# Optimization experiments

Measured on AMD Instinct MI355X. Metric: run time of the kernel, lower is better.

The kernel has to match this reference:

```python
import jax, jax.numpy as jnp
import numpy as np

B, IMG, TXT, N, FF, HID, C, E = 1024, 512, 300, 14, 2048, 128, 14, 182
D = IMG + TXT  # 812, transformer d_model


def setup_inputs() -> dict:
    key = jax.random.key(0)
    ks = jax.random.split(key, 12)
    r = lambda k, s, sc=0.02: (jax.random.normal(k, s, jnp.float32) * sc)
    return {
        "img_feat": jax.random.normal(ks[0], (B, IMG), jnp.float32),
        "word_embeds": jax.random.normal(ks[1], (N, TXT), jnp.float32),
        "edge_index": jax.random.randint(ks[2], (2, E), 0, N, jnp.int32),
        "in_proj_w": r(ks[3], (3 * D, D)),
        "in_proj_b": jnp.zeros((3 * D,), jnp.float32),
        "out_proj_w": r(ks[4], (D, D)),
        "out_proj_b": jnp.zeros((D,), jnp.float32),
        "ln1_g": jnp.ones((D,), jnp.float32), "ln1_b": jnp.zeros((D,), jnp.float32),
        "ln2_g": jnp.ones((D,), jnp.float32), "ln2_b": jnp.zeros((D,), jnp.float32),
        "ffn_w1": r(ks[5], (D, FF)), "ffn_b1": jnp.zeros((FF,), jnp.float32),
        "ffn_w2": r(ks[6], (FF, D)), "ffn_b2": jnp.zeros((D,), jnp.float32),
        "gcn1_w": r(ks[7], (D, HID)), "gcn1_b": jnp.zeros((HID,), jnp.float32),
        "gcn2_w": r(ks[8], (HID, HID)), "gcn2_b": jnp.zeros((HID,), jnp.float32),
        "lin_w": r(ks[9], (HID, C)), "lin_b": jnp.zeros((C,), jnp.float32),
    }


def layer_norm(x, g, b, eps=1e-5):
    mu = x.mean(-1, keepdims=True)
    var = ((x - mu) ** 2).mean(-1, keepdims=True)
    return (x - mu) * jax.lax.rsqrt(var + eps) * g + b


def gcn_conv(x, edge_index, W, b, n_nodes):
    # PyG GCNConv: add self loops, symmetric normalization, x @ W then scatter-add.
    # x: (B, N, F_in); gather/scatter along node axis (node_dim=-2).
    src, dst = edge_index[0], edge_index[1]
    loop = jnp.arange(n_nodes, dtype=src.dtype)
    src = jnp.concatenate([src, loop])
    dst = jnp.concatenate([dst, loop])
    deg = jnp.zeros((n_nodes,), x.dtype).at[dst].add(1.0)
    dinv = jnp.where(deg > 0, deg ** -0.5, 0.0)
    ew = dinv[src] * dinv[dst]                       # (E+N,)
    h = x @ W                                        # (B, N, F_out)
    msg = h[:, src, :] * ew[None, :, None]           # gather neighbors
    out = jnp.zeros_like(h).at[:, dst, :].add(msg)   # scatter-aggregate
    return out + b


def reference(img_feat, word_embeds, edge_index,
              in_proj_w, in_proj_b, out_proj_w, out_proj_b,
              ln1_g, ln1_b, ln2_g, ln2_b,
              ffn_w1, ffn_b1, ffn_w2, ffn_b2,
              gcn1_w, gcn1_b, gcn2_w, gcn2_b, lin_w, lin_b):
    # Broadcast image feature across the 14 label nodes; concat word embeddings.
    node = jnp.concatenate([
        jnp.broadcast_to(img_feat[:, None, :], (B, N, IMG)),
        jnp.broadcast_to(word_embeds[None, :, :], (B, N, TXT)),
    ], axis=-1)                                      # (B, N, D)

    # torch TransformerEncoderLayer, batch_first=False, nhead=1, post-norm, relu.
    # Input (B, N, D) is interpreted as (seq=B, batch=N, D): attention over dim 0.
    qkv = node @ in_proj_w.T + in_proj_b
    q, k, v = jnp.split(qkv, 3, axis=-1)             # each (B, N, D)
    scale = 1.0 / jnp.sqrt(jnp.asarray(D, node.dtype))
    scores = jnp.einsum('lnd,mnd->nlm', q, k) * scale  # (N, B, B)
    attn = jax.nn.softmax(scores, axis=-1)
    ao = jnp.einsum('nlm,mnd->lnd', attn, v)           # (B, N, D)
    ao = ao @ out_proj_w.T + out_proj_b
    x = layer_norm(node + ao, ln1_g, ln1_b)
    ff = jax.nn.relu(x @ ffn_w1 + ffn_b1) @ ffn_w2 + ffn_b2
    x = layer_norm(x + ff, ln2_g, ln2_b)               # (B, N, D)

    # Two GCNConv layers over the 14-node label graph (batched over B).
    x = jax.nn.relu(gcn_conv(x, edge_index, gcn1_w, gcn1_b, N))
    x = gcn_conv(x, edge_index, gcn2_w, gcn2_b, N)
    x = jax.nn.relu(x.mean(axis=1))                    # mean over nodes -> (B, HID)
    return x @ lin_w + lin_b                           # (B, C)
```

## Files before the change

kernel.cpp:

```cpp
#include <hip/hip_runtime.h>
#include <math.h>

#define B_    1024
#define IMG_  512
#define TXT_  300
#define NN_   14
#define FF_   2048
#define HID_  128
#define CC_   14
#define EE_   182
#define DD_   812
#define D3_   2436
#define BNR_  14336
#define KP_   832
#define TXP_  320
#define AROWS_ 1152

typedef __bf16 bf16x8 __attribute__((ext_vector_type(8)));
typedef float  f32x4  __attribute__((ext_vector_type(4)));
typedef unsigned short u16;

__device__ __forceinline__ u16 f2bf(float f) {
    union { float f; unsigned u; } v; v.f = f;
    unsigned r = v.u + 0x7FFFu + ((v.u >> 16) & 1u);
    return (u16)(r >> 16);
}
__device__ __forceinline__ float bf2f(u16 h) {
    union { unsigned u; float f; } v; v.u = ((unsigned)h) << 16; return v.f;
}

__device__ __forceinline__ void gload_lds16(const u16* g, u16* l) {
    __builtin_amdgcn_global_load_lds(
        (const __attribute__((address_space(1))) void*)g,
        (__attribute__((address_space(3))) void*)l, 16, 0, 0);
}

#define OFF_IMGB  0ULL
#define OFF_WIB   1048576ULL
#define OFF_WORDB 3543040ULL
#define OFF_WITX  3624960ULL
#define OFF_GB    0ULL
#define OFF_EBUF  29360128ULL
#define OFF_AVOT  33611776ULL
#define OFF_WOB   35446784ULL
#define OFF_HB    0ULL
#define OFF_PB    58720256ULL
#define OFF_X1B   82001920ULL
#define OFF_YB    105857024ULL
#define OFF_W1T   129712128ULL
#define OFF_W2T   133120000ULL
#define OFF_AQB   152420352ULL
#define OFF_TVB   158307552ULL
#define OFF_CO    158520544ULL
#define OFF_Z     158566016ULL
#define OFF_ADJ   158623360ULL
#define OFF_WG1T  158624384ULL
#define OFF_WG2T  158837376ULL

__device__ __forceinline__ void gemm_epi(
    float v, int rm, int cn, int epi,
    float* __restrict__ Cf, int ldc, u16* __restrict__ Cb, int ldcb,
    const float* __restrict__ bias)
{
    if (epi == 0) Cf[(size_t)rm * ldc + cn] = v;
    else if (epi == 1) { v += bias[cn]; v = v > 0.f ? v : 0.f;
                    Cb[(size_t)rm * ldcb + cn] = f2bf(v); }
    else if (epi == 2) Cf[(size_t)rm * ldc + cn] =
                    v + bias[cn] + bf2f(Cb[(size_t)rm * ldcb + cn]);
    else if (epi == 3) Cb[(size_t)rm * ldcb + cn] = f2bf(v);
    else if (epi == 4) { int bs = cn / DD_, cc = cn - bs * DD_;
                    Cb[(size_t)bs * (AROWS_ * KP_) + (size_t)rm * KP_ + cc] = f2bf(v); }
    else if (epi == 5) { float invz = 1.0f / bias[rm];
                    Cb[(size_t)rm * ldcb + cn] = f2bf(v * invz); }
    else if (epi == 6) Cf[(size_t)rm * ldc + cn] = v + bias[cn];
    else if (epi == 7) { const u16* rx = (const u16*)Cf;
                    Cb[(size_t)rm * ldcb + cn] =
                        f2bf(v + bias[cn] + bf2f(rx[(size_t)rm * ldc + cn])); }
    else if (epi == 8) {
        float t = v + bias[cn];
        if (cn < DD_) Cb[(size_t)(1024 + rm) * KP_ + cn] = f2bf(t);
        else if (cn >= 2 * DD_)
            ((u16*)Cf)[(size_t)rm * KP_ + (cn - 2 * DD_)] = f2bf(t);
    }
}

__device__ __forceinline__ void gemm256_body(
    const u16* __restrict__ A, int lda,
    const u16* __restrict__ Bm, int ldb,
    int M, int N, int K, float scale,
    float* __restrict__ Cf, int ldc,
    u16* __restrict__ Cb, int ldcb,
    const float* __restrict__ bias,
    int nxt, int epi, int id)
{
    __shared__ __align__(16) u16 As[4][8192];
    __shared__ __align__(16) u16 Bs[4][8192];
    const int tid = threadIdx.x;
    const int bx = id % nxt, by = id / nxt;
    const int row0 = by << 8, col0 = bx << 8;
    const int lane = tid & 63, wv = tid >> 6;
    const int wm = (wv >> 2) << 7;
    const int wn = (wv & 3) << 6;
    const int fr = lane & 15, qd = lane >> 4;

    int aoff[8], boff[4];
    #pragma unroll
    for (int mi = 0; mi < 8; ++mi) {
        int r = wm + mi * 16 + fr;
        aoff[mi] = r * 32 + ((qd ^ ((r >> 1) & 3)) << 3);
    }
    #pragma unroll
    for (int ni = 0; ni < 4; ++ni) {
        int r = wn + ni * 16 + fr;
        boff[ni] = r * 32 + ((qd ^ ((r >> 1) & 3)) << 3);
    }

    const int i0 = tid, i1 = 512 + tid;
    const int r0 = i0 >> 2, r1 = i1 >> 2;
    const int c0 = ((i0 & 3) ^ ((r0 >> 1) & 3)) << 3;
    const int c1 = ((i1 & 3) ^ ((r1 >> 1) & 3)) << 3;
    const u16* Ag0 = A  + (size_t)(row0 + r0) * lda + c0;
    const u16* Ag1 = A  + (size_t)(row0 + r1) * lda + c1;
    const u16* Bg0 = Bm + (size_t)(col0 + r0) * ldb + c0;
    const u16* Bg1 = Bm + (size_t)(col0 + r1) * ldb + c1;
    const int lb0 = wv * 512;
    const int lb1 = 4096 + wv * 512;

    f32x4 acc[8][4] = {};
    const int T = K >> 5;

    #pragma unroll
    for (int p = 0; p < 3; ++p) {
        const int ko = p << 5;
        gload_lds16(Ag0 + ko, &As[p][lb0]);
        gload_lds16(Ag1 + ko, &As[p][lb1]);
        gload_lds16(Bg0 + ko, &Bs[p][lb0]);
        gload_lds16(Bg1 + ko, &Bs[p][lb1]);
    }
    __builtin_amdgcn_sched_barrier(0);
    asm volatile("s_waitcnt vmcnt(8)");
    __builtin_amdgcn_sched_barrier(0);
    __builtin_amdgcn_s_barrier();
    __builtin_amdgcn_sched_barrier(0);

    for (int t = 0; t < T; ++t) {
        const int slot = t & 3;
        const u16* as = &As[slot][0];
        const u16* bs = &Bs[slot][0];
        const int ns = (t + 3) & 3;
        const int ko = (t + 3) << 5;
        const bool pf = (t + 3 < T);

        bf16x8 a[8];
        #pragma unroll
        for (int mi = 0; mi < 8; ++mi)
            a[mi] = *(const bf16x8*)(as + aoff[mi]);
        bf16x8 b0 = *(const bf16x8*)(bs + boff[0]);
        bf16x8 b1 = *(const bf16x8*)(bs + boff[1]);
        if (pf) {
            gload_lds16(Ag0 + ko, &As[ns][lb0]);
            gload_lds16(Ag1 + ko, &As[ns][lb1]);
        }
        __builtin_amdgcn_sched_barrier(0);
        __builtin_amdgcn_s_barrier();
        __builtin_amdgcn_sched_barrier(0);
        __builtin_amdgcn_s_setprio(1);
        #pragma unroll
        for (int mi = 0; mi < 8; ++mi) {
            acc[mi][0] = __builtin_amdgcn_mfma_f32_16x16x32_bf16(
                a[mi], b0, acc[mi][0], 0, 0, 0);
            acc[mi][1] = __builtin_amdgcn_mfma_f32_16x16x32_bf16(
                a[mi], b1, acc[mi][1], 0, 0, 0);
        }
        __builtin_amdgcn_s_setprio(0);
        __builtin_amdgcn_sched_barrier(0);
        __builtin_amdgcn_s_barrier();
        __builtin_amdgcn_sched_barrier(0);

        bf16x8 b2 = *(const bf16x8*)(bs + boff[2]);
        bf16x8 b3 = *(const bf16x8*)(bs + boff[3]);
        if (pf) {
            gload_lds16(Bg0 + ko, &Bs[ns][lb0]);
            gload_lds16(Bg1 + ko, &Bs[ns][lb1]);
        }
        __builtin_amdgcn_sched_barrier(0);
        if (t < T - 3) asm volatile("s_waitcnt vmcnt(8)");
        else           asm volatile("s_waitcnt vmcnt(0)");
        __builtin_amdgcn_sched_barrier(0);
        __builtin_amdgcn_s_barrier();
        __builtin_amdgcn_sched_barrier(0);
        __builtin_amdgcn_s_setprio(1);
        #pragma unroll
        for (int mi = 0; mi < 8; ++mi) {
            acc[mi][2] = __builtin_amdgcn_mfma_f32_16x16x32_bf16(
                a[mi], b2, acc[mi][2], 0, 0, 0);
            acc[mi][3] = __builtin_amdgcn_mfma_f32_16x16x32_bf16(
                a[mi], b3, acc[mi][3], 0, 0, 0);
        }
        __builtin_amdgcn_s_setprio(0);
        __builtin_amdgcn_sched_barrier(0);
        __builtin_amdgcn_s_barrier();
        __builtin_amdgcn_sched_barrier(0);
    }

    #pragma unroll
    for (int mi = 0; mi < 8; ++mi) {
        #pragma unroll
        for (int i = 0; i < 4; ++i) {
            int rm = row0 + wm + mi * 16 + qd * 4 + i;
            if (rm >= M) continue;
            #pragma unroll
            for (int ni = 0; ni < 4; ++ni) {
                int cn = col0 + wn + ni * 16 + fr;
                if (cn >= N) continue;
                gemm_epi(acc[mi][ni][i] * scale, rm, cn, epi, Cf, ldc, Cb, ldcb, bias);
            }
        }
    }
}

template<int EPI>
__global__ __launch_bounds__(512, 2)
void bgemm256(const u16* __restrict__ A, int lda,
              const u16* __restrict__ Bm, int ldb,
              int M, int N, int K, float scale,
              float* __restrict__ Cf, int ldc,
              u16* __restrict__ Cb, int ldcb,
              const float* __restrict__ bias,
              int nxt)
{
    const int g8 = (int)gridDim.x >> 3;
    const int id = (int)blockIdx.x;
    const int w = (id & 7) * g8 + (id >> 3);
    gemm256_body(A, lda, Bm, ldb, M, N, K, scale, Cf, ldc, Cb, ldcb, bias,
                 nxt, EPI, w);
}

__device__ __forceinline__ void gemm_body8(
    const u16* __restrict__ A, int lda,
    const u16* __restrict__ Bm, int ldb,
    int M, int N, int K, float scale,
    float* __restrict__ Cf, int ldc,
    u16* __restrict__ Cb, int ldcb,
    const float* __restrict__ bias,
    int nxt, int swiz, int epi, int id)
{
    __shared__ __align__(16) u16 As[2][128 * 32];
    __shared__ __align__(16) u16 Bs[2][128 * 32];
    const int tid = threadIdx.x;
    int bx, by;
    if (swiz) { int r8 = id & 7; int q = id >> 3; bx = q % nxt; by = (q / nxt) * 8 + r8; }
    else      { bx = id % nxt; by = id / nxt; }
    const int row0 = by * 128, col0 = bx * 128;
    const int lane = tid & 63, wv = tid >> 6;
    const int wm = (wv >> 1) * 32, wn = (wv & 1) * 64;
    const int fr = lane & 15, qd = lane >> 4;

    const int s_b0  = wv * 512;
    const int s_row = tid >> 2;
    const int s_ko  = (tid & 3) * 8;
    const u16* Arow = A  + (size_t)(row0 + s_row) * lda + s_ko;
    const u16* Brow = Bm + (size_t)(col0 + s_row) * ldb + s_ko;

    f32x4 acc[2][4] = {};

    const int T = K >> 5;
    gload_lds16(Arow, &As[0][s_b0]);
    gload_lds16(Brow, &Bs[0][s_b0]);

    for (int i = 0; i < T; ++i) {
        __syncthreads();
        const int cur = i & 1;
        if (i + 1 < T) {
            const int ko = (i + 1) << 5;
            gload_lds16(Arow + ko, &As[cur ^ 1][s_b0]);
            gload_lds16(Brow + ko, &Bs[cur ^ 1][s_b0]);
        }
        bf16x8 af[2], bg[4];
        #pragma unroll
        for (int j = 0; j < 2; ++j)
            af[j] = *(const bf16x8*)&As[cur][(wm + j * 16 + fr) * 32 + qd * 8];
        #pragma unroll
        for (int j = 0; j < 4; ++j)
            bg[j] = *(const bf16x8*)&Bs[cur][(wn + j * 16 + fr) * 32 + qd * 8];
        #pragma unroll
        for (int mi = 0; mi < 2; ++mi)
            #pragma unroll
            for (int ni = 0; ni < 4; ++ni)
                acc[mi][ni] = __builtin_amdgcn_mfma_f32_16x16x32_bf16(
                    af[mi], bg[ni], acc[mi][ni], 0, 0, 0);
    }

    #pragma unroll
    for (int mi = 0; mi < 2; ++mi) {
        #pragma unroll
        for (int i = 0; i < 4; ++i) {
            int rm = row0 + wm + mi * 16 + qd * 4 + i;
            if (rm >= M) continue;
            #pragma unroll
            for (int ni = 0; ni < 4; ++ni) {
                int cn = col0 + wn + ni * 16 + fr;
                if (cn >= N) continue;
                gemm_epi(acc[mi][ni][i] * scale, rm, cn, epi, Cf, ldc, Cb, ldcb, bias);
            }
        }
    }
}

struct GDesc {
    const u16* A; const u16* B; float* Cf; u16* Cb; const float* bias;
    int lda, ldb, ldc, ldcb, M, N, K, epi, nxt, swiz, blk0;
    float scale;
};
struct TDesc { const float* src; u16* dst; int srs, drs, rows, cols, padrows, rt, nblk; };
struct MPack { GDesc g[3]; TDesc t[2]; const int* ei; float* Adj; int ng, gtot, nt; };

__device__ __forceinline__ void castT_body(TDesc T, int id)
{
    __shared__ float t[32][33];
    const int bx = id % T.rt, by = id / T.rt;
    const int r0 = bx * 32, c0 = by * 32;
    const int tx = threadIdx.x & 31, ty = threadIdx.x >> 5;
    #pragma unroll
    for (int k = 0; k < 2; ++k) {
        int r = r0 + ty + k * 16, c = c0 + tx;
        t[ty + k * 16][tx] = (r < T.rows && c < T.cols) ? T.src[(size_t)r * T.srs + c] : 0.f;
    }
    __syncthreads();
    #pragma unroll
    for (int k = 0; k < 2; ++k) {
        int c = c0 + ty + k * 16, r = r0 + tx;
        if (c < T.cols && r < T.padrows)
            T.dst[(size_t)c * T.drs + r] = f2bf(t[tx][ty + k * 16]);
    }
}

__device__ __forceinline__ void adj_body(const int* __restrict__ ei, float* __restrict__ Adj)
{
    __shared__ float degS[NN_], dinvS[NN_], adjS[NN_ * NN_];
    const int tid = threadIdx.x;
    if (tid < NN_) degS[tid] = 1.f;
    if (tid < NN_ * NN_) adjS[tid] = 0.f;
    __syncthreads();
    int s = 0, d = 0;
    if (tid < EE_) { s = ei[tid]; d = ei[EE_ + tid]; atomicAdd(&degS[d], 1.f); }
    __syncthreads();
    if (tid < NN_) dinvS[tid] = rsqrtf(degS[tid]);
    __syncthreads();
    if (tid < EE_) atomicAdd(&adjS[d * NN_ + s], dinvS[s] * dinvS[d]);
    if (tid < NN_) atomicAdd(&adjS[tid * NN_ + tid], dinvS[tid] * dinvS[tid]);
    __syncthreads();
    if (tid < NN_ * NN_) Adj[tid] = adjS[tid];
    if (tid < 16) {
        float sum = 0.f;
        if (tid < NN_)
            for (int j = 0; j < NN_; ++j) sum += adjS[j * NN_ + tid];
        Adj[NN_ * NN_ + tid] = sum / (float)NN_;
    }
}

__global__ __launch_bounds__(512, 6)
void kern_mix(MPack p)
{
    int id = blockIdx.x;
    if (id < p.gtot) {
        int si = 0;
        for (int s = 1; s < p.ng; ++s) if (id >= p.g[s].blk0) si = s;
        GDesc D = p.g[si];
        gemm_body8(D.A, D.lda, D.B, D.ldb, D.M, D.N, D.K, D.scale,
                   D.Cf, D.ldc, D.Cb, D.ldcb, D.bias, D.nxt, D.swiz, D.epi,
                   id - D.blk0);
        return;
    }
    id -= p.gtot;
    for (int s = 0; s < p.nt; ++s) {
        if (id < p.t[s].nblk) { castT_body(p.t[s], id); return; }
        id -= p.t[s].nblk;
    }
    if (id == 0 && p.ei) adj_body(p.ei, p.Adj);
}

struct CDesc { const float* src; u16* dst; int srs, drs, dcols, scols; };
struct CPack { CDesc d[9]; unsigned cum[10]; int n; };

__global__ void kern_mcast(CPack p)
{
    unsigned idx = blockIdx.x * 256 + threadIdx.x;
    int si = -1;
    for (int s = 0; s < p.n; ++s)
        if (idx >= p.cum[s] && idx < p.cum[s + 1]) { si = s; break; }
    if (si < 0) return;
    CDesc D = p.d[si];
    unsigned k = idx - p.cum[si];
    int r = k / D.dcols, c = k - r * D.dcols;
    D.dst[(size_t)r * D.drs + c] =
        (c < D.scols) ? f2bf(D.src[(size_t)r * D.srs + c]) : (u16)0;
}

__global__ __launch_bounds__(256) void kern_eG(const float* __restrict__ S,
    u16* __restrict__ Gb, float* __restrict__ Z)
{
    __shared__ float red[256];
    __shared__ u16 ews[NN_ * 1024];
    const int l = blockIdx.x, tid = threadIdx.x;
    const int lane = tid & 63, wv = tid >> 6;

    const float* wraw = S + 1024 * 1024;
    for (int z = wv; z < NN_; z += 4) {
        const float* r = wraw + z * 1024;
        float vv[16], mx = -1e30f;
        #pragma unroll
        for (int j = 0; j < 16; ++j) { vv[j] = r[lane + 64 * j]; mx = fmaxf(mx, vv[j]); }
        #pragma unroll
        for (int off = 32; off > 0; off >>= 1) mx = fmaxf(mx, __shfl_down(mx, off));
        mx = __shfl(mx, 0);
        #pragma unroll
        for (int j = 0; j < 16; ++j)
            ews[z * 1024 + lane + 64 * j] = f2bf(expf(vv[j] - mx));
    }
    const float* row = S + (size_t)l * 1024;
    float m = -1e30f;
    #pragma unroll
    for (int k = 0; k < 4; ++k) m = fmaxf(m, row[tid + 256 * k]);
    red[tid] = m; __syncthreads();
    for (int s = 128; s > 0; s >>= 1) {
        if (tid < s) red[tid] = fmaxf(red[tid], red[tid + s]);
        __syncthreads();
    }
    m = red[0];
    float ev[16];
    #pragma unroll
    for (int j = 0; j < 16; ++j) ev[j] = expf(row[lane + 64 * j] - m);
    u16* gr = Gb + (size_t)l * NN_ * 1024;
    for (int z = wv; z < NN_; z += 4) {
        const u16* er = &ews[z * 1024];
        float s = 0.f;
        #pragma unroll
        for (int j = 0; j < 16; ++j) {
            float pv = ev[j] * bf2f(er[lane + 64 * j]);
            gr[(size_t)z * 1024 + lane + 64 * j] = f2bf(pv);
            s += pv;
        }
        #pragma unroll
        for (int off = 32; off > 0; off >>= 1) s += __shfl_down(s, off);
        if (lane == 0) Z[l * NN_ + z] = s;
    }
}

__global__ __launch_bounds__(256) void kern_ln1(
    const float* __restrict__ img, const float* __restrict__ word,
    const u16* __restrict__ Pb,
    const float* __restrict__ co, const float* __restrict__ g,
    const float* __restrict__ bta, u16* __restrict__ Xb)
{
    __shared__ float buf[DD_];
    __shared__ float red[256];
    __shared__ float stats[2];
    int row = blockIdx.x;
    int b = row / NN_, n = row - b * NN_;
    const u16* pr = Pb + (size_t)row * DD_;
    const float* cr = co + n * DD_;
    float s = 0.f;
    for (int d = threadIdx.x; d < DD_; d += 256) {
        float v = (d < IMG_) ? img[(size_t)b * IMG_ + d] : word[n * TXT_ + d - IMG_];
        v += bf2f(pr[d]) + cr[d];
        buf[d] = v; s += v;
    }
    red[threadIdx.x] = s; __syncthreads();
    for (int t = 128; t > 0; t >>= 1) {
        if (threadIdx.x < t) red[threadIdx.x] += red[threadIdx.x + t];
        __syncthreads();
    }
    if (threadIdx.x == 0) stats[0] = red[0] / DD_;
    __syncthreads();
    float mu = stats[0], s2 = 0.f;
    for (int d = threadIdx.x; d < DD_; d += 256) { float t = buf[d] - mu; s2 += t * t; }
    red[threadIdx.x] = s2; __syncthreads();
    for (int t = 128; t > 0; t >>= 1) {
        if (threadIdx.x < t) red[threadIdx.x] += red[threadIdx.x + t];
        __syncthreads();
    }
    if (threadIdx.x == 0) stats[1] = rsqrtf(red[0] / DD_ + 1e-5f);
    __syncthreads();
    float rstd = stats[1];
    u16* xb = Xb + (size_t)row * KP_;
    for (int d = threadIdx.x; d < DD_; d += 256)
        xb[d] = f2bf((buf[d] - mu) * rstd * g[d] + bta[d]);
    for (int d = DD_ + threadIdx.x; d < KP_; d += 256) xb[d] = 0;
}

#define X2S_ 840
#define G1S_ 136
__global__ __launch_bounds__(256, 4)
void kern_gcn(const u16* __restrict__ Yb,
              const float* __restrict__ g2v, const float* __restrict__ bt2,
              const u16* __restrict__ Wg1T, const float* __restrict__ bg1,
              const u16* __restrict__ Wg2T, const float* __restrict__ bg2,
              const float* __restrict__ Wl,  const float* __restrict__ bl,
              const float* __restrict__ AdjW, float* __restrict__ out)
{
    __shared__ __align__(16) u16 x2s[16 * X2S_];
    __shared__ __align__(16) float h1s[16 * 132];
    __shared__ float adj_s[NN_ * NN_];
    __shared__ float colw_s[16];
    __shared__ float pool_s[HID_];
    u16* g1s = x2s;
    const int b = blockIdx.x, tid = threadIdx.x;
    const int lane = tid & 63, wv = tid >> 6;
    const int fr = lane & 15, qd = lane >> 4;

    if (tid < NN_ * NN_) adj_s[tid] = AdjW[tid];
    if (tid >= NN_ * NN_ && tid < NN_ * NN_ + 16) colw_s[tid - NN_ * NN_] = AdjW[tid];
    for (int k = tid; k < 2 * X2S_; k += 256) x2s[14 * X2S_ + k] = 0;
    for (int k = tid; k < 14 * (X2S_ - DD_); k += 256) {
        int j = k / (X2S_ - DD_), c = k - j * (X2S_ - DD_);
        x2s[j * X2S_ + DD_ + c] = 0;
    }

    for (int j = wv; j < NN_; j += 4) {
        const u16* yr = Yb + (size_t)(b * NN_ + j) * KP_;
        float vv[13], s = 0.f;
        #pragma unroll
        for (int k = 0; k < 13; ++k) {
            int d = lane + 64 * k;
            float v = (d < DD_) ? bf2f(yr[d]) : 0.f;
            vv[k] = v; s += v;
        }
        #pragma unroll
        for (int off = 32; off > 0; off >>= 1) s += __shfl_down(s, off);
        s = __shfl(s, 0);
        float mu = s / (float)DD_, s2 = 0.f;
        #pragma unroll
        for (int k = 0; k < 13; ++k) {
            int d = lane + 64 * k;
            float t = (d < DD_) ? vv[k] - mu : 0.f;
            s2 += t * t;
        }
        #pragma unroll
        for (int off = 32; off > 0; off >>= 1) s2 += __shfl_down(s2, off);
        s2 = __shfl(s2, 0);
        float rstd = rsqrtf(s2 / (float)DD_ + 1e-5f);
        #pragma unroll
        for (int k = 0; k < 13; ++k) {
            int d = lane + 64 * k;
            if (d < DD_)
                x2s[j * X2S_ + d] = f2bf((vv[k] - mu) * rstd * g2v[d] + bt2[d]);
        }
    }
    __syncthreads();

    {
        f32x4 acc[2] = {{}, {}};
        const u16* wp0 = Wg1T + (size_t)(wv * 32 + fr) * KP_ + qd * 8;
        const u16* wp1 = wp0 + (size_t)16 * KP_;
        bf16x8 bc0 = *(const bf16x8*)wp0;
        bf16x8 bc1 = *(const bf16x8*)wp1;
        for (int k0 = 0; k0 < KP_; k0 += 32) {
            bf16x8 bn0 = bc0, bn1 = bc1;
            if (k0 + 32 < KP_) {
                bn0 = *(const bf16x8*)(wp0 + k0 + 32);
                bn1 = *(const bf16x8*)(wp1 + k0 + 32);
            }
            bf16x8 af = *(const bf16x8*)&x2s[fr * X2S_ + k0 + qd * 8];
            acc[0] = __builtin_amdgcn_mfma_f32_16x16x32_bf16(af, bc0, acc[0], 0, 0, 0);
            acc[1] = __builtin_amdgcn_mfma_f32_16x16x32_bf16(af, bc1, acc[1], 0, 0, 0);
            bc0 = bn0; bc1 = bn1;
        }
        #pragma unroll
        for (int t = 0; t < 2; ++t)
            #pragma unroll
            for (int i = 0; i < 4; ++i)
                h1s[(qd * 4 + i) * 132 + wv * 32 + t * 16 + fr] = acc[t][i];
    }
    __syncthreads();

    {
        const int f = tid & 127, jj = (tid >> 7) * 7;
        #pragma unroll
        for (int j = 0; j < 7; ++j) {
            float s = bg1[f];
            #pragma unroll
            for (int i = 0; i < NN_; ++i)
                s = fmaf(adj_s[(jj + j) * NN_ + i], h1s[i * 132 + f], s);
            g1s[(jj + j) * G1S_ + f] = f2bf(s > 0.f ? s : 0.f);
        }
        for (int k = tid; k < 2 * G1S_; k += 256) g1s[14 * G1S_ + k] = 0;
    }
    __syncthreads();

    {
        f32x4 acc[2] = {{}, {}};
        const u16* wp0 = Wg2T + (size_t)(wv * 32 + fr) * HID_ + qd * 8;
        const u16* wp1 = wp0 + (size_t)16 * HID_;
        bf16x8 bc0 = *(const bf16x8*)wp0;
        bf16x8 bc1 = *(const bf16x8*)wp1;
        for (int k0 = 0; k0 < HID_; k0 += 32) {
            bf16x8 bn0 = bc0, bn1 = bc1;
            if (k0 + 32 < HID_) {
                bn0 = *(const bf16x8*)(wp0 + k0 + 32);
                bn1 = *(const bf16x8*)(wp1 + k0 + 32);
            }
            bf16x8 af = *(const bf16x8*)&g1s[fr * G1S_ + k0 + qd * 8];
            acc[0] = __builtin_amdgcn_mfma_f32_16x16x32_bf16(af, bc0, acc[0], 0, 0, 0);
            acc[1] = __builtin_amdgcn_mfma_f32_16x16x32_bf16(af, bc1, acc[1], 0, 0, 0);
            bc0 = bn0; bc1 = bn1;
        }
        #pragma unroll
        for (int t = 0; t < 2; ++t) {
            float s = 0.f;
            #pragma unroll
            for (int i = 0; i < 4; ++i) s += colw_s[qd * 4 + i] * acc[t][i];
            s += __shfl_xor(s, 16);
            s += __shfl_xor(s, 32);
            if (qd == 0) {
                int f = wv * 32 + t * 16 + fr;
                float p = s + bg2[f];
                pool_s[f] = p > 0.f ? p : 0.f;
            }
        }
    }
    __syncthreads();

    if (tid < CC_) {
        float s = bl[tid];
        #pragma unroll 8
        for (int f = 0; f < HID_; ++f)
            s = fmaf(pool_s[f], Wl[(size_t)f * CC_ + tid], s);
        out[(size_t)b * CC_ + tid] = s;
    }
}

extern "C" void kernel_launch(void* const* d_in, const int* in_sizes, int n_in,
                              void* d_out, int out_size, void* d_ws, size_t ws_size,
                              hipStream_t stream)
{
    const float* img  = (const float*)d_in[0];
    const float* word = (const float*)d_in[1];
    const int*   ei   = (const int*)d_in[2];
    const float* Wi   = (const float*)d_in[3];
    const float* bi   = (const float*)d_in[4];
    const float* Wo   = (const float*)d_in[5];
    const float* bo   = (const float*)d_in[6];
    const float* g1   = (const float*)d_in[7];
    const float* bt1  = (const float*)d_in[8];
    const float* g2   = (const float*)d_in[9];
    const float* bt2  = (const float*)d_in[10];
    const float* W1   = (const float*)d_in[11];
    const float* bf1  = (const float*)d_in[12];
    const float* W2   = (const float*)d_in[13];
    const float* bf2  = (const float*)d_in[14];
    const float* Wg1  = (const float*)d_in[15];
    const float* bg1  = (const float*)d_in[16];
    const float* Wg2  = (const float*)d_in[17];
    const float* bg2  = (const float*)d_in[18];
    const float* Wl   = (const float*)d_in[19];
    const float* bl   = (const float*)d_in[20];
    float* out = (float*)d_out;

    char* ws = (char*)d_ws;
    u16*   imgb = (u16*)  (ws + OFF_IMGB);
    u16*   Wib  = (u16*)  (ws + OFF_WIB);
    u16*   wordb= (u16*)  (ws + OFF_WORDB);
    u16*   WiTX = (u16*)  (ws + OFF_WITX);
    u16*   Gb   = (u16*)  (ws + OFF_GB);
    float* Ebuf = (float*)(ws + OFF_EBUF);
    u16*   AvoT = (u16*)  (ws + OFF_AVOT);
    u16*   Wob  = (u16*)  (ws + OFF_WOB);
    u16*   Hb   = (u16*)  (ws + OFF_HB);
    u16*   Pb   = (u16*)  (ws + OFF_PB);
    u16*   X1b  = (u16*)  (ws + OFF_X1B);
    u16*   Yb   = (u16*)  (ws + OFF_YB);
    u16*   W1T  = (u16*)  (ws + OFF_W1T);
    u16*   W2T  = (u16*)  (ws + OFF_W2T);
    u16*   Aqb  = (u16*)  (ws + OFF_AQB);
    u16*   Akb  = Aqb + AROWS_ * KP_;
    u16*   Avb  = Aqb + 2 * AROWS_ * KP_;
    u16*   Tvb  = (u16*)  (ws + OFF_TVB);
    float* co   = (float*)(ws + OFF_CO);
    float* Zb   = (float*)(ws + OFF_Z);
    float* Adj  = (float*)(ws + OFF_ADJ);
    u16*   Wg1T = (u16*)  (ws + OFF_WG1T);
    u16*   Wg2T = (u16*)  (ws + OFF_WG2T);

    const float scl = 1.0f / sqrtf((float)DD_);

    {
        CPack p; p.n = 9;
        unsigned c = 0;
        auto seg = [&](int i, const float* s, int srs, u16* d, int drs,
                       int rows, int dcols, int scols) {
            p.d[i] = { s, d, srs, drs, dcols, scols };
            p.cum[i] = c; c += (unsigned)rows * dcols;
        };
        seg(0, img,        IMG_, imgb,  IMG_, B_,   IMG_, IMG_);
        seg(1, Wi,         DD_,  Wib,   IMG_, D3_,  IMG_, IMG_);
        seg(2, word,       TXT_, wordb, TXP_, NN_,  TXP_, TXT_);
        seg(3, Wi + IMG_,  DD_,  WiTX,  TXP_, D3_,  TXP_, TXT_);
        seg(4, Wo,         DD_,  Wob,   KP_,  DD_,  KP_,  DD_);
        seg(5, nullptr, 0, Aqb + DD_,                    KP_, 1038, 20, 0);
        seg(6, nullptr, 0, Aqb + AROWS_ * KP_ + DD_,     KP_, 1024, 20, 0);
        seg(7, nullptr, 0, Aqb + 2 * AROWS_ * KP_ + DD_, KP_, 1024, 20, 0);
        seg(8, nullptr, 0, Tvb + DD_,                    KP_, NN_,  20, 0);
        p.cum[9] = c;
        kern_mcast<<<(c + 255) / 256, 256, 0, stream>>>(p);
    }

    {
        MPack p{};
        p.ng = 2; p.gtot = 180;
        p.g[0] = { wordb, WiTX, (float*)Tvb, Aqb, bi,
                   TXP_, TXP_, 0, 0, NN_, D3_, TXP_, 8, 20, 0, 0, 1.f };
        p.g[1] = { imgb, Wib, nullptr, Aqb, nullptr,
                   IMG_, IMG_, 0, 0, B_, D3_, IMG_, 4, 20, 1, 20, 1.f };
        p.nt = 2;
        p.t[0] = { Wg1, Wg1T, HID_, KP_,  DD_,  HID_, KP_,  26, 26 * 4 };
        p.t[1] = { Wg2, Wg2T, HID_, HID_, HID_, HID_, HID_, 4,  4 * 4 };
        p.ei = ei; p.Adj = Adj;
        kern_mix<<<180 + 104 + 16 + 1, 512, 0, stream>>>(p);
    }

    {
        MPack p{};
        p.ng = 3; p.gtot = 135;
        p.g[0] = { Aqb, Akb, Ebuf, nullptr, nullptr,
                   KP_, KP_, 1024, 0, 1024 + NN_, 1024, KP_, 0, 8, 0, 0, scl };
        p.g[1] = { Wob, Avb, nullptr, AvoT, nullptr,
                   KP_, KP_, 0, 1024, DD_, B_, KP_, 3, 8, 0, 72, 1.f };
        p.g[2] = { Tvb, Wob, co, nullptr, bo,
                   KP_, KP_, DD_, 0, NN_, DD_, KP_, 6, 7, 0, 128, 1.f };
        p.nt = 2;
        p.t[0] = { W1, W1T, FF_, KP_, DD_, FF_, KP_, 26, 26 * 64 };
        p.t[1] = { W2, W2T, DD_, FF_, FF_, DD_, FF_, 64, 64 * 26 };
        p.ei = nullptr; p.Adj = nullptr;
        kern_mix<<<135 + 1664 + 1664, 512, 0, stream>>>(p);
    }

    kern_eG<<<1024, 256, 0, stream>>>(Ebuf, Gb, Zb);

    bgemm256<5><<<56 * 4, 512, 0, stream>>>(Gb, 1024, AvoT, 1024,
        BNR_, DD_, 1024, 1.f, nullptr, 0, Pb, DD_, Zb, 4);

    kern_ln1<<<BNR_, 256, 0, stream>>>(img, word, Pb, co, g1, bt1, X1b);

    bgemm256<1><<<56 * 8, 512, 0, stream>>>(X1b, KP_, W1T, KP_,
        BNR_, FF_, KP_, 1.f, nullptr, 0, Hb, FF_, bf1, 8);
    bgemm256<7><<<56 * 4, 512, 0, stream>>>(Hb, FF_, W2T, FF_,
        BNR_, DD_, FF_, 1.f, (float*)X1b, KP_, Yb, KP_, bf2, 4);

    kern_gcn<<<B_, 256, 0, stream>>>(Yb, g2, bt2, Wg1T, bg1, Wg2T, bg2,
                                     Wl, bl, Adj, out);
}
```

Measured before the change: 478.4 us.

## Add 128x128 double-buffered GEMM with grouped tile swizzle for attention-out and FFN1

Adds a new 128x128-tile MFMA GEMM kernel with 256 threads, two LDS buffers of 32-wide K slices, and an optional row-grouped block swizzle that improves L2 reuse. The attention-value GEMM and the first FFN GEMM now use it instead of the 256x256 kernel. The aim is to launch more blocks for better occupancy and load balance across CUs, since the 256-tile grid of 224 or 448 blocks may underfill the device. The cost is less data reuse per tile and more global traffic. The FFN2 GEMM keeps the old kernel.

After: 459.4 us. 4.0% less time.

```diff
diff --git a/kernel.cpp b/kernel.cpp
--- a/kernel.cpp
+++ b/kernel.cpp
@@ -82,6 +82,97 @@
         else if (cn >= 2 * DD_)
             ((u16*)Cf)[(size_t)rm * KP_ + (cn - 2 * DD_)] = f2bf(t);
     }
+}
+
+__device__ __forceinline__ void gemm_body4(
+    const u16* __restrict__ A, int lda,
+    const u16* __restrict__ Bm, int ldb,
+    int M, int N, int K, float scale,
+    float* __restrict__ Cf, int ldc,
+    u16* __restrict__ Cb, int ldcb,
+    const float* __restrict__ bias,
+    int nxt, int swiz, int epi, int id)
+{
+    __shared__ __align__(16) u16 As[2][128 * 32];
+    __shared__ __align__(16) u16 Bs[2][128 * 32];
+    const int tid = threadIdx.x;
+    int bx, by;
+    if (swiz) { int r8 = id & 7; int q = id >> 3; bx = q % nxt; by = (q / nxt) * 8 + r8; }
+    else      { bx = id % nxt; by = id / nxt; }
+    const int row0 = by * 128, col0 = bx * 128;
+    const int lane = tid & 63, wv = tid >> 6;
+    const int wm = (wv >> 1) * 64, wn = (wv & 1) * 64;
+    const int fr = lane & 15, qd = lane >> 4;
+
+    const int s_r0  = (wv * 64 + lane) >> 2;
+    const int s_ko  = (lane & 3) * 8;
+    const int s_b0  = (wv * 64) * 8;
+    const u16* Arow0 = A  + (size_t)(row0 + s_r0) * lda + s_ko;
+    const u16* Arow1 = A  + (size_t)(row0 + s_r0 + 64) * lda + s_ko;
+    const u16* Brow0 = Bm + (size_t)(col0 + s_r0) * ldb + s_ko;
+    const u16* Brow1 = Bm + (size_t)(col0 + s_r0 + 64) * ldb + s_ko;
+
+    f32x4 acc[4][4] = {};
+
+    const int T = K >> 5;
+    gload_lds16(Arow0, &As[0][s_b0]);
+    gload_lds16(Arow1, &As[0][s_b0 + 2048]);
+    gload_lds16(Brow0, &Bs[0][s_b0]);
+    gload_lds16(Brow1, &Bs[0][s_b0 + 2048]);
+
+    for (int i = 0; i < T; ++i) {
+        __syncthreads();
+        const int cur = i & 1;
+        if (i + 1 < T) {
+            const int nb = cur ^ 1;
+            const int ko = (i + 1) << 5;
+            gload_lds16(Arow0 + ko, &As[nb][s_b0]);
+            gload_lds16(Arow1 + ko, &As[nb][s_b0 + 2048]);
+            gload_lds16(Brow0 + ko, &Bs[nb][s_b0]);
+            gload_lds16(Brow1 + ko, &Bs[nb][s_b0 + 2048]);
+        }
+        bf16x8 af[4], bg[4];
+        #pragma unroll
+        for (int j = 0; j < 4; ++j) {
+            af[j] = *(const bf16x8*)&As[cur][(wm + j * 16 + fr) * 32 + qd * 8];
+            bg[j] = *(const bf16x8*)&Bs[cur][(wn + j * 16 + fr) * 32 + qd * 8];
+        }
+        #pragma unroll
+        for (int mi = 0; mi < 4; ++mi)
+            #pragma unroll
+            for (int ni = 0; ni < 4; ++ni)
+                acc[mi][ni] = __builtin_amdgcn_mfma_f32_16x16x32_bf16(
+                    af[mi], bg[ni], acc[mi][ni], 0, 0, 0);
+    }
+
+    #pragma unroll
+    for (int mi = 0; mi < 4; ++mi) {
+        #pragma unroll
+        for (int i = 0; i < 4; ++i) {
+            int rm = row0 + wm + mi * 16 + qd * 4 + i;
+            if (rm >= M) continue;
+            #pragma unroll
+            for (int ni = 0; ni < 4; ++ni) {
+                int cn = col0 + wn + ni * 16 + fr;
+                if (cn >= N) continue;
+                gemm_epi(acc[mi][ni][i] * scale, rm, cn, epi, Cf, ldc, Cb, ldcb, bias);
+            }
+        }
+    }
+}
+
+template<int EPI>
+__global__ __launch_bounds__(256, 4)
+void bgemm(const u16* __restrict__ A, int lda,
+           const u16* __restrict__ Bm, int ldb,
+           int M, int N, int K, float scale,
+           float* __restrict__ Cf, int ldc,
+           u16* __restrict__ Cb, int ldcb,
+           const float* __restrict__ bias,
+           int nxt, int swiz)
+{
+    gemm_body4(A, lda, Bm, ldb, M, N, K, scale, Cf, ldc, Cb, ldcb, bias,
+               nxt, swiz, EPI, blockIdx.x);
 }
 
 __device__ __forceinline__ void gemm256_body(
@@ -737,13 +828,14 @@
 
     kern_eG<<<1024, 256, 0, stream>>>(Ebuf, Gb, Zb);
 
-    bgemm256<5><<<56 * 4, 512, 0, stream>>>(Gb, 1024, AvoT, 1024,
-        BNR_, DD_, 1024, 1.f, nullptr, 0, Pb, DD_, Zb, 4);
+    bgemm<5><<<7 * 112, 256, 0, stream>>>(Gb, 1024, AvoT, 1024,
+        BNR_, DD_, 1024, 1.f, nullptr, 0, Pb, DD_, Zb, 7, 1);
 
     kern_ln1<<<BNR_, 256, 0, stream>>>(img, word, Pb, co, g1, bt1, X1b);
 
-    bgemm256<1><<<56 * 8, 512, 0, stream>>>(X1b, KP_, W1T, KP_,
-        BNR_, FF_, KP_, 1.f, nullptr, 0, Hb, FF_, bf1, 8);
+    bgemm<1><<<16 * 112, 256, 0, stream>>>(X1b, KP_, W1T, KP_,
+        BNR_, FF_, KP_, 1.f, nullptr, 0, Hb, FF_, bf1, 16, 1);
+
     bgemm256<7><<<56 * 4, 512, 0, stream>>>(Hb, FF_, W2T, FF_,
         BNR_, DD_, FF_, 1.f, (float*)X1b, KP_, Yb, KP_, bf2, 4);
 
```
